# Performance work log

Hardware: AMD Instinct MI355X
Metric: run time of the kernel (lower is better)

The kernel has to match this reference:

```python
import jax, jax.numpy as jnp
import numpy as np

D = 1024      # d_model
H = 16        # nhead
DH = D // H   # d_head = 64
DC = D // 4   # d_compress = 256
HID = 2048    # dim_feedforward (SwiGLU hidden)
G = 2         # num_groups
EPG = 4       # experts_per_gp
E = G * EPG   # num_experts = 8
TOPK = 2
EPS = 1e-6
B, T = 2, 2048


def _rope_sincos(t, dh):
    inv_freq = 1.0 / (10000.0 ** (jnp.arange(0, dh, 2, dtype=jnp.float32) / dh))
    ang = jnp.arange(t, dtype=jnp.float32)[:, None] * inv_freq[None, :]  # [T, dh/2]
    return jnp.sin(ang), jnp.cos(ang)


def _apply_rope(x, sin, cos):
    # x: [B, H, T, DH]; sin/cos: [T, DH/2] broadcast over B,H
    x1 = x[..., ::2]
    x2 = x[..., 1::2]
    r = jnp.stack([x1 * cos - x2 * sin, x1 * sin + x2 * cos], axis=-1)
    return r.reshape(x.shape)


def _swiglu(x):
    a, b = jnp.split(x, 2, axis=-1)
    return jax.nn.silu(a) * b


def _rmsnorm(x, w):
    return x * jax.lax.rsqrt(jnp.mean(x * x, axis=-1, keepdims=True) + EPS) * w


def reference(src, Wq, Wk_c, Wv_c, Wk, Wv, Wo,
              W_shared_in, W_shared_out, W1_shared, W2_experts,
              Wg_gate, We_gate, group_bias, expert_bias, norm1_w, norm2_w):
    Bb, Tt, C = src.shape
    # ---- Latent attention (K/V compressed to d_c then re-expanded) ----
    q = (src @ Wq).reshape(Bb, Tt, H, DH).transpose(0, 2, 1, 3)
    k = ((src @ Wk_c) @ Wk).reshape(Bb, Tt, H, DH).transpose(0, 2, 1, 3)
    v = ((src @ Wv_c) @ Wv).reshape(Bb, Tt, H, DH).transpose(0, 2, 1, 3)
    sin, cos = _rope_sincos(Tt, DH)
    q = _apply_rope(q, sin, cos)
    k = _apply_rope(k, sin, cos)
    attn = jnp.einsum('bhqd,bhkd->bhqk', q, k) / np.sqrt(DH).astype(np.float32)
    attn = jax.nn.softmax(attn, axis=-1)
    sa = jnp.einsum('bhqk,bhkd->bhqd', attn, v)
    sa = sa.transpose(0, 2, 1, 3).reshape(Bb, Tt, C) @ Wo
    x = _rmsnorm(src + sa, norm1_w)

    # ---- Hierarchical MoE FFN ----
    S = Bb * Tt
    flat = x.reshape(S, C)
    shared = _swiglu(flat @ W_shared_in) @ W_shared_out          # [S, C]
    g_probs = jax.nn.softmax(flat @ Wg_gate + group_bias, -1)    # [S, G]
    g_idx = jnp.argmax(g_probs, axis=-1)                          # [S]
    e_logits = flat @ We_gate + expert_bias                       # [S, E]
    e_group = jnp.arange(E) // EPG
    in_group = e_group[None, :] == g_idx[:, None]                 # [S, E]
    e_probs = jax.nn.softmax(jnp.where(in_group, e_logits, -jnp.inf), -1)
    g_prob = jnp.take_along_axis(g_probs, g_idx[:, None], axis=1)  # [S, 1]
    p_expert = e_probs * g_prob
    topv, topi = jax.lax.top_k(p_expert, TOPK)                    # [S, K]
    # dense combine weights: zero for non-selected experts (same math as dispatch loop)
    w = jnp.zeros((S, E), flat.dtype).at[jnp.arange(S)[:, None], topi].set(topv)
    h = _swiglu(flat @ W1_shared)                                 # [S, HID] (w1 shared by all experts)
    routed = jnp.zeros_like(shared)
    for e in range(E):  # fixed small expert count
        routed = routed + (h @ W2_experts[e]) * w[:, e:e + 1]
    out = x + (shared + routed).reshape(Bb, Tt, C)
    return _rmsnorm(out, norm2_w)


def setup_inputs() -> dict:
    key = jax.random.key(0)
    ks = jax.random.split(key, 14)
    s = 0.02
    return {
        'src': jax.random.normal(ks[0], (B, T, D), jnp.float32),
        'Wq': jax.random.normal(ks[1], (D, D), jnp.float32) * s,
        'Wk_c': jax.random.normal(ks[2], (D, DC), jnp.float32) * s,
        'Wv_c': jax.random.normal(ks[3], (D, DC), jnp.float32) * s,
        'Wk': jax.random.normal(ks[4], (DC, D), jnp.float32) * s,
        'Wv': jax.random.normal(ks[5], (DC, D), jnp.float32) * s,
        'Wo': jax.random.normal(ks[6], (D, D), jnp.float32) * s,
        'W_shared_in': jax.random.normal(ks[7], (D, 2 * HID), jnp.float32) * s,
        'W_shared_out': jax.random.normal(ks[8], (HID, D), jnp.float32) * s,
        'W1_shared': jax.random.normal(ks[9], (D, 2 * HID), jnp.float32) * s,
        'W2_experts': jax.random.normal(ks[10], (E, HID, D), jnp.float32) * s,
        'Wg_gate': jax.random.normal(ks[11], (D, G), jnp.float32) * s,
        'We_gate': jax.random.normal(ks[12], (D, E), jnp.float32) * s,
        'group_bias': jnp.zeros((G,), jnp.float32),
        'expert_bias': jnp.zeros((E,), jnp.float32),
        'norm1_w': jnp.ones((D,), jnp.float32),
        'norm2_w': jnp.ones((D,), jnp.float32),
    }
```

## Files before the change

### kernel.cpp

```cpp
#include <hip/hip_runtime.h>
#include <math.h>

#define D_    1024
#define H_    16
#define DH_   64
#define DC_   256
#define HID_  2048
#define E_    8
#define B_    2
#define T_    2048
#define S_    4096
#define EPS_  1e-6f
#define QKVW_ 3072

typedef unsigned short u16;
typedef short bf16x8 __attribute__((ext_vector_type(8)));
typedef float f32x4 __attribute__((ext_vector_type(4)));

__device__ __forceinline__ float b2f(u16 u) {
    return __uint_as_float(((unsigned int)u) << 16);
}
__device__ __forceinline__ u16 f2b(float f) {
    unsigned int u = __float_as_uint(f);
    u += 0x7FFF + ((u >> 16) & 1);
    return (u16)(u >> 16);
}
__device__ __forceinline__ void g2l16(const u16* g, u16* l) {
    __builtin_amdgcn_global_load_lds(
        (const __attribute__((address_space(1))) void*)g,
        (__attribute__((address_space(3))) void*)l, 16, 0, 0);
}

__global__ __launch_bounds__(256) void conv_t(const float* __restrict__ in,
                                              u16* __restrict__ out,
                                              int K, int N,
                                              long inZ, long outZ, int perm) {
    in  += (long)blockIdx.z * inZ;
    out += (long)blockIdx.z * outZ;
    __shared__ float t[32][33];
    const int n0 = blockIdx.x * 32, k0 = blockIdx.y * 32;
    int src_n0 = n0;
    if (perm) {
        int t64 = n0 >> 6;
        src_n0 = ((n0 & 63) == 0) ? t64 * 32 : (N / 2 + t64 * 32);
    }
    const int tx = threadIdx.x & 31, ty = threadIdx.x >> 5;
#pragma unroll
    for (int i = 0; i < 4; i++)
        t[ty + 8 * i][tx] = in[(long)(k0 + ty + 8 * i) * N + src_n0 + tx];
    __syncthreads();
#pragma unroll
    for (int i = 0; i < 4; i++)
        out[(long)(n0 + ty + 8 * i) * K + k0 + tx] = f2b(t[tx][ty + 8 * i]);
}

__global__ __launch_bounds__(256) void vt_conv(const u16* __restrict__ qkv,
                                               u16* __restrict__ vt) {
    __shared__ u16 t[32][34];
    const int bh = blockIdx.z;
    const int b = bh >> 4, h = bh & 15;
    const int t0 = blockIdx.x * 32, d0 = blockIdx.y * 32;
    const int tx = threadIdx.x & 31, ty = threadIdx.x >> 5;
#pragma unroll
    for (int i = 0; i < 4; i++)
        t[ty + 8 * i][tx] =
            qkv[((long)b * T_ + t0 + ty + 8 * i) * QKVW_ + 2048 + h * 64 + d0 + tx];
    __syncthreads();
#pragma unroll
    for (int i = 0; i < 4; i++)
        vt[((long)bh * 64 + d0 + ty + 8 * i) * T_ + t0 + tx] = t[tx][ty + 8 * i];
}

__global__ __launch_bounds__(256) void convert_bf16(const float* __restrict__ in,
                                                    u16* __restrict__ out, int n4) {
    int i = blockIdx.x * 256 + threadIdx.x;
    if (i >= n4) return;
    float4 f = ((const float4*)in)[i];
    ushort4 o;
    o.x = f2b(f.x); o.y = f2b(f.y); o.z = f2b(f.z); o.w = f2b(f.w);
    ((ushort4*)out)[i] = o;
}

template<int OUTMODE>
__global__ __launch_bounds__(256) void gemm_bf16(const u16* __restrict__ A,
                                                 const u16* __restrict__ Bt,
                                                 void* __restrict__ Cp,
                                                 int N, int K, int ldo,
                                                 void* __restrict__ Cp2) {
    __shared__ u16 As[128 * 32];
    __shared__ u16 Bs[128 * 32];
    const int tid  = threadIdx.x;
    const int lane = tid & 63;
    const int wv   = tid >> 6;
    const int wm   = wv >> 1, wn = wv & 1;
    const long row0 = (long)blockIdx.y * 128;
    const long col0 = (long)blockIdx.x * 128;
    const int Klocal = K / gridDim.z;
    const long koff  = (long)blockIdx.z * Klocal;

    f32x4 acc[4][4];
#pragma unroll
    for (int i = 0; i < 4; i++)
#pragma unroll
        for (int j = 0; j < 4; j++) acc[i][j] = (f32x4){0.f, 0.f, 0.f, 0.f};

    const int sr = tid >> 2;
    const int sc = (tid & 3) << 3;
    const u16* Ag  = A  + (row0 + sr) * (long)K + koff + sc;
    const u16* Ag2 = Ag + 64 * (long)K;
    const u16* Bg  = Bt + (col0 + sr) * (long)K + koff + sc;
    const u16* Bg2 = Bg + 64 * (long)K;
    u16* lA  = As + tid * 8;
    u16* lA2 = As + 2048 + tid * 8;
    u16* lB  = Bs + tid * 8;
    u16* lB2 = Bs + 2048 + tid * 8;

    const int fl = lane & 15;
    const int fk = (lane >> 4) << 3;
    const u16* ArA = As + (wm * 64 + fl) * 32 + fk;
    const u16* BrB = Bs + (wn * 64 + fl) * 32 + fk;

    for (int k0 = 0; k0 < Klocal; k0 += 32) {
        __syncthreads();
        g2l16(Ag + k0, lA);
        g2l16(Ag2 + k0, lA2);
        g2l16(Bg + k0, lB);
        g2l16(Bg2 + k0, lB2);
        __syncthreads();
        bf16x8 af[4], bfr[4];
#pragma unroll
        for (int mi = 0; mi < 4; mi++) af[mi]  = *(const bf16x8*)(ArA + mi * 512);
#pragma unroll
        for (int ni = 0; ni < 4; ni++) bfr[ni] = *(const bf16x8*)(BrB + ni * 512);
#pragma unroll
        for (int mi = 0; mi < 4; mi++)
#pragma unroll
            for (int ni = 0; ni < 4; ni++)
                acc[mi][ni] = __builtin_amdgcn_mfma_f32_16x16x32_bf16(
                    af[mi], bfr[ni], acc[mi][ni], 0, 0, 0);
    }

    const int cr = (lane >> 4) << 2;
    const int cc = lane & 15;
#pragma unroll
    for (int mi = 0; mi < 4; mi++) {
#pragma unroll
        for (int r = 0; r < 4; r++) {
            long grow = row0 + wm * 64 + mi * 16 + cr + r;
            if (OUTMODE == 3) {
                u16* outb = (u16*)Cp + (long)(blockIdx.x >> 5) * S_ * HID_;
                u16* hrow = outb + grow * ldo + (blockIdx.x & 31) * 64 + wn * 32;
#pragma unroll
                for (int ni = 0; ni < 2; ni++) {
                    float a = acc[mi][ni][r], b = acc[mi][ni + 2][r];
                    float sig = 1.f / (1.f + __expf(-a));
                    hrow[ni * 16 + cc] = f2b(a * sig * b);
                }
            } else {
#pragma unroll
                for (int ni = 0; ni < 4; ni++) {
                    long gcol = col0 + wn * 64 + ni * 16 + cc;
                    float v = acc[mi][ni][r];
                    if (OUTMODE == 1)      ((u16*)Cp)[grow * ldo + gcol] = f2b(v);
                    else if (OUTMODE == 2) ((u16*)Cp)[gcol * ldo + grow] = f2b(v);
                    else {
                        float* basep = (float*)(blockIdx.z ? Cp2 : Cp);
                        basep[grow * ldo + gcol] = v;
                    }
                }
            }
        }
    }
}

__global__ __launch_bounds__(256) void routed_gemm(const u16* __restrict__ Hh,
                                                   const u16* __restrict__ W2T,
                                                   const int* __restrict__ list,
                                                   const float* __restrict__ wlist,
                                                   const int* __restrict__ bases,
                                                   const int* __restrict__ counts,
                                                   float* __restrict__ Cout) {
    const int e    = blockIdx.y >> 5;
    const int tile = blockIdx.y & 31;
    const int cnt  = counts[e];
    if (tile * 128 >= cnt) return;
    const int base = bases[e];

    __shared__ u16 As[128 * 32];
    __shared__ u16 Bs[128 * 32];
    __shared__ int   toks[128];
    __shared__ float wrow[128];

    const int tid = threadIdx.x;
    if (tid < 128) {
        int ridx = tile * 128 + tid;
        if (ridx < cnt) { toks[tid] = list[base + ridx]; wrow[tid] = wlist[base + ridx]; }
        else            { toks[tid] = -1;                wrow[tid] = 0.f; }
    }
    __syncthreads();

    const int lane = tid & 63;
    const int wv   = tid >> 6;
    const int wm   = wv >> 1, wn = wv & 1;
    const long col0 = (long)blockIdx.x * 128;

    f32x4 acc[4][4];
#pragma unroll
    for (int i = 0; i < 4; i++)
#pragma unroll
        for (int j = 0; j < 4; j++) acc[i][j] = (f32x4){0.f, 0.f, 0.f, 0.f};

    const int sr = tid >> 2;
    const int sc = (tid & 3) << 3;
    const int t1 = toks[sr], t2 = toks[sr + 64];
    const u16* Ag  = Hh + (long)(t1 < 0 ? 0 : t1) * HID_ + sc;
    const u16* Ag2 = Hh + (long)(t2 < 0 ? 0 : t2) * HID_ + sc;
    const u16* Bg  = W2T + (long)e * D_ * HID_ + (col0 + sr) * (long)HID_ + sc;
    const u16* Bg2 = Bg + 64 * (long)HID_;
    u16* lA  = As + tid * 8;
    u16* lA2 = As + 2048 + tid * 8;
    u16* lB  = Bs + tid * 8;
    u16* lB2 = Bs + 2048 + tid * 8;

    const int fl = lane & 15;
    const int fk = (lane >> 4) << 3;
    const u16* ArA = As + (wm * 64 + fl) * 32 + fk;
    const u16* BrB = Bs + (wn * 64 + fl) * 32 + fk;

    for (int k0 = 0; k0 < HID_; k0 += 32) {
        __syncthreads();
        g2l16(Ag + k0, lA);
        g2l16(Ag2 + k0, lA2);
        g2l16(Bg + k0, lB);
        g2l16(Bg2 + k0, lB2);
        __syncthreads();
        bf16x8 af[4], bfr[4];
#pragma unroll
        for (int mi = 0; mi < 4; mi++) af[mi]  = *(const bf16x8*)(ArA + mi * 512);
#pragma unroll
        for (int ni = 0; ni < 4; ni++) bfr[ni] = *(const bf16x8*)(BrB + ni * 512);
#pragma unroll
        for (int mi = 0; mi < 4; mi++)
#pragma unroll
            for (int ni = 0; ni < 4; ni++)
                acc[mi][ni] = __builtin_amdgcn_mfma_f32_16x16x32_bf16(
                    af[mi], bfr[ni], acc[mi][ni], 0, 0, 0);
    }

    const int cr = (lane >> 4) << 2;
    const int cc = lane & 15;
#pragma unroll
    for (int mi = 0; mi < 4; mi++) {
#pragma unroll
        for (int r = 0; r < 4; r++) {
            int rr = wm * 64 + mi * 16 + cr + r;
            int tk = toks[rr];
            if (tk < 0) continue;
            float wvw = wrow[rr];
            float* crow = Cout + (long)tk * D_ + col0 + wn * 64;
#pragma unroll
            for (int ni = 0; ni < 4; ni++)
                atomicAdd(crow + ni * 16 + cc, acc[mi][ni][r] * wvw);
        }
    }
}

__global__ __launch_bounds__(256) void rope_table(float2* __restrict__ tab) {
    int idx = blockIdx.x * 256 + threadIdx.x;
    int t = idx >> 5, i = idx & 31;
    float ang = (float)t * powf(10000.f, -(float)i / 32.f);
    float sn, cs;
    sincosf(ang, &sn, &cs);
    tab[idx] = make_float2(sn, cs);
}

__global__ __launch_bounds__(256) void rope_apply(u16* __restrict__ qkv,
                                                  const float2* __restrict__ tab) {
    long p = (long)blockIdx.x * 256 + threadIdx.x;
    int s  = (int)(p >> 8);
    int c8 = (int)(p & 255) << 3;
    int t  = s & (T_ - 1);
    const float2* tp = tab + t * 32 + ((c8 & 63) >> 1);
    u16* px = qkv + (long)s * QKVW_ + c8;
    bf16x8 v = *(const bf16x8*)px;
    bf16x8 o;
#pragma unroll
    for (int j = 0; j < 4; j++) {
        float x1 = b2f((u16)v[2 * j]), x2 = b2f((u16)v[2 * j + 1]);
        float2 sc = tp[j];
        o[2 * j]     = (short)f2b(x1 * sc.y - x2 * sc.x);
        o[2 * j + 1] = (short)f2b(x1 * sc.x + x2 * sc.y);
    }
    *(bf16x8*)px = o;
}

__global__ __launch_bounds__(512) void attn_kernel(const u16* __restrict__ qkv,
                                                   const u16* __restrict__ vtg,
                                                   u16* __restrict__ sab) {
    __shared__ u16 Ks[128 * 64];
    __shared__ u16 Vs[64 * 128];
    __shared__ u16 Ps[8][16 * 128];
    const int tid  = threadIdx.x;
    const int lane = tid & 63;
    const int w    = tid >> 6;
    const int bh = blockIdx.y;
    const int b  = bh >> 4, h = bh & 15;
    const long tok0 = (long)b * T_ + blockIdx.x * 128;
    const int fl = lane & 15;
    const int fq = lane >> 4;

    bf16x8 qf0, qf1;
    {
        const u16* qp = qkv + (tok0 + w * 16 + fl) * QKVW_ + h * 64 + fq * 8;
        qf0 = *(const bf16x8*)qp;
        qf1 = *(const bf16x8*)(qp + 32);
    }

    const u16* kb0 = qkv + ((long)b * T_) * QKVW_ + 1024 + h * 64;
    const u16* vb0 = vtg + ((long)bh * 64) * T_;

    float m_[4], l_[4];
    f32x4 oacc[4];
#pragma unroll
    for (int i = 0; i < 4; i++) {
        m_[i] = -1e30f; l_[i] = 0.f;
        oacc[i] = (f32x4){0.f, 0.f, 0.f, 0.f};
    }

    for (int kt = 0; kt < T_ / 128; kt++) {
        __syncthreads();
#pragma unroll
        for (int ps = 0; ps < 2; ps++) {
            int i = tid + ps * 512;
            int row = i >> 3, gg = i & 7;
            g2l16(kb0 + (long)(kt * 128 + row) * QKVW_ + ((gg ^ (row & 7)) << 3),
                  Ks + i * 8);
        }
#pragma unroll
        for (int ps = 0; ps < 2; ps++) {
            int i = tid + ps * 512;
            int row = i >> 4, gg = i & 15;
            g2l16(vb0 + (long)row * T_ + kt * 128 + ((gg ^ (row & 15)) << 3),
                  Vs + i * 8);
        }
        __syncthreads();

        f32x4 sacc[8];
#pragma unroll
        for (int ni = 0; ni < 8; ni++) sacc[ni] = (f32x4){0.f, 0.f, 0.f, 0.f};
#pragma unroll
        for (int ks = 0; ks < 2; ks++) {
            bf16x8 qq = ks ? qf1 : qf0;
#pragma unroll
            for (int ni = 0; ni < 8; ni++) {
                bf16x8 kf = *(const bf16x8*)(Ks + (ni * 16 + fl) * 64 +
                                             (((ks * 4 + fq) ^ (fl & 7)) << 3));
                sacc[ni] = __builtin_amdgcn_mfma_f32_16x16x32_bf16(qq, kf, sacc[ni], 0, 0, 0);
            }
        }

        float rmax[4];
#pragma unroll
        for (int r = 0; r < 4; r++) {
            float mm = sacc[0][r];
#pragma unroll
            for (int ni = 1; ni < 8; ni++) mm = fmaxf(mm, sacc[ni][r]);
            rmax[r] = mm * 0.125f;
        }
#pragma unroll
        for (int off = 1; off < 16; off <<= 1)
#pragma unroll
            for (int r = 0; r < 4; r++) rmax[r] = fmaxf(rmax[r], __shfl_xor(rmax[r], off));
        float alpha[4], psum[4];
#pragma unroll
        for (int r = 0; r < 4; r++) {
            float nm = fmaxf(m_[r], rmax[r]);
            alpha[r] = __expf(m_[r] - nm);
            m_[r] = nm;
            psum[r] = 0.f;
        }
        u16* pst = Ps[w];
#pragma unroll
        for (int ni = 0; ni < 8; ni++) {
            int colg = ni * 2 + (fl >> 3);
            int cl   = fl & 7;
#pragma unroll
            for (int r = 0; r < 4; r++) {
                int row = fq * 4 + r;
                float p = __expf(sacc[ni][r] * 0.125f - m_[r]);
                psum[r] += p;
                pst[row * 128 + ((colg ^ (row & 15)) << 3) + cl] = f2b(p);
            }
        }
#pragma unroll
        for (int off = 1; off < 16; off <<= 1)
#pragma unroll
            for (int r = 0; r < 4; r++) psum[r] += __shfl_xor(psum[r], off);
#pragma unroll
        for (int r = 0; r < 4; r++) l_[r] = l_[r] * alpha[r] + psum[r];
#pragma unroll
        for (int ni = 0; ni < 4; ni++)
#pragma unroll
            for (int r = 0; r < 4; r++) oacc[ni][r] *= alpha[r];

#pragma unroll
        for (int ks = 0; ks < 4; ks++) {
            bf16x8 pf = *(const bf16x8*)(pst + fl * 128 +
                                         (((ks * 4 + fq) ^ fl) << 3));
#pragma unroll
            for (int ni = 0; ni < 4; ni++) {
                bf16x8 vf = *(const bf16x8*)(Vs + (ni * 16 + fl) * 128 +
                                             (((ks * 4 + fq) ^ fl) << 3));
                oacc[ni] = __builtin_amdgcn_mfma_f32_16x16x32_bf16(pf, vf, oacc[ni], 0, 0, 0);
            }
        }
    }

#pragma unroll
    for (int r = 0; r < 4; r++) {
        float inv = 1.f / l_[r];
        u16* op = sab + (tok0 + w * 16 + fq * 4 + r) * D_ + h * 64 + fl;
#pragma unroll
        for (int ni = 0; ni < 4; ni++) op[ni * 16] = f2b(oacc[ni][r] * inv);
    }
}

template<int BF>
__global__ __launch_bounds__(256) void rmsnorm_res(const float* __restrict__ a,
                                                   const float* __restrict__ b,
                                                   const float* __restrict__ b2,
                                                   const float* __restrict__ w,
                                                   float* __restrict__ outf,
                                                   u16* __restrict__ outb) {
    const int s = blockIdx.x;
    const float* ar = a + (long)s * D_;
    const float* br = b + (long)s * D_;
    const float* cr2 = b2 + (long)s * D_;
    float y[4];
    float ss = 0.f;
#pragma unroll
    for (int kx = 0; kx < 4; kx++) {
        int j = threadIdx.x + kx * 256;
        y[kx] = ar[j] + br[j] + cr2[j];
        ss += y[kx] * y[kx];
    }
    __shared__ float red[4];
#pragma unroll
    for (int off = 32; off > 0; off >>= 1) ss += __shfl_down(ss, off);
    int lane = threadIdx.x & 63, wv = threadIdx.x >> 6;
    if (lane == 0) red[wv] = ss;
    __syncthreads();
    float tot = red[0] + red[1] + red[2] + red[3];
    float scl = rsqrtf(tot / (float)D_ + EPS_);
    float* orow = outf + (long)s * D_;
#pragma unroll
    for (int kx = 0; kx < 4; kx++) {
        int j = threadIdx.x + kx * 256;
        float v = y[kx] * scl * w[j];
        orow[j] = v;
        if (BF) outb[(long)s * D_ + j] = f2b(v);
    }
}

__global__ __launch_bounds__(256) void gate_kernel(const float* __restrict__ x,
                                                   const float* __restrict__ Wg,
                                                   const float* __restrict__ We,
                                                   const float* __restrict__ gb,
                                                   const float* __restrict__ eb,
                                                   int* __restrict__ tok_e,
                                                   float* __restrict__ tok_w) {
    const int wave = threadIdx.x >> 6;
    const int lane = threadIdx.x & 63;
    const int s = blockIdx.x * 4 + wave;
    const float* xr = x + (long)s * D_;
    float g0 = 0.f, g1 = 0.f;
    float ee[8];
#pragma unroll
    for (int e = 0; e < 8; e++) ee[e] = 0.f;
    for (int j = lane; j < D_; j += 64) {
        float xv = xr[j];
        g0 += xv * Wg[j * 2 + 0];
        g1 += xv * Wg[j * 2 + 1];
#pragma unroll
        for (int e = 0; e < 8; e++) ee[e] += xv * We[j * 8 + e];
    }
#pragma unroll
    for (int off = 32; off > 0; off >>= 1) {
        g0 += __shfl_down(g0, off);
        g1 += __shfl_down(g1, off);
#pragma unroll
        for (int e = 0; e < 8; e++) ee[e] += __shfl_down(ee[e], off);
    }
    if (lane == 0) {
        g0 += gb[0];
        g1 += gb[1];
        int gidx = (g1 > g0) ? 1 : 0;
        float gm = fmaxf(g0, g1);
        float p0 = expf(g0 - gm), p1 = expf(g1 - gm);
        float gprob = (gidx ? p1 : p0) / (p0 + p1);
        int base = gidx * 4;
        float pe[4];
        float em = -1e30f;
#pragma unroll
        for (int i = 0; i < 4; i++) {
            pe[i] = ee[base + i] + eb[base + i];
            em = fmaxf(em, pe[i]);
        }
        float sum = 0.f;
#pragma unroll
        for (int i = 0; i < 4; i++) { pe[i] = expf(pe[i] - em); sum += pe[i]; }
        float inv = gprob / sum;
#pragma unroll
        for (int i = 0; i < 4; i++) pe[i] *= inv;
        int i1 = 0;
        for (int i = 1; i < 4; i++) if (pe[i] > pe[i1]) i1 = i;
        int i2 = -1;
        for (int i = 0; i < 4; i++) {
            if (i == i1) continue;
            if (i2 < 0 || pe[i] > pe[i2]) i2 = i;
        }
        tok_e[s * 2 + 0] = base + i1;
        tok_e[s * 2 + 1] = base + i2;
        tok_w[s * 2 + 0] = pe[i1];
        tok_w[s * 2 + 1] = pe[i2];
    }
}

__global__ __launch_bounds__(256) void route_build(const int* __restrict__ tok_e,
                                                   const float* __restrict__ tok_w,
                                                   int* __restrict__ counts_g,
                                                   int* __restrict__ bases_g,
                                                   int* __restrict__ list,
                                                   float* __restrict__ wlist) {
    __shared__ int cnt[E_], bas[E_], cur[E_];
    const int tid = threadIdx.x;
    if (tid < E_) cnt[tid] = 0;
    __syncthreads();
    for (int i = tid; i < 2 * S_; i += 256) atomicAdd(&cnt[tok_e[i]], 1);
    __syncthreads();
    if (tid == 0) {
        int acc = 0;
        for (int e = 0; e < E_; e++) { bas[e] = acc; cur[e] = acc; acc += cnt[e]; }
    }
    __syncthreads();
    if (tid < E_) { counts_g[tid] = cnt[tid]; bases_g[tid] = bas[tid]; }
    for (int i = tid; i < 2 * S_; i += 256) {
        int e = tok_e[i];
        int p = atomicAdd(&cur[e], 1);
        list[p] = i >> 1;
        wlist[p] = tok_w[i];
    }
}

extern "C" void kernel_launch(void* const* d_in, const int* in_sizes, int n_in,
                              void* d_out, int out_size, void* d_ws, size_t ws_size,
                              hipStream_t stream) {
    const float* src  = (const float*)d_in[0];
    const float* Wq   = (const float*)d_in[1];
    const float* Wk_c = (const float*)d_in[2];
    const float* Wv_c = (const float*)d_in[3];
    const float* Wk   = (const float*)d_in[4];
    const float* Wv   = (const float*)d_in[5];
    const float* Wo   = (const float*)d_in[6];
    const float* Wsin = (const float*)d_in[7];
    const float* Wsout= (const float*)d_in[8];
    const float* W1   = (const float*)d_in[9];
    const float* W2   = (const float*)d_in[10];
    const float* Wg   = (const float*)d_in[11];
    const float* We   = (const float*)d_in[12];
    const float* gb   = (const float*)d_in[13];
    const float* eb   = (const float*)d_in[14];
    const float* n1w  = (const float*)d_in[15];
    const float* n2w  = (const float*)d_in[16];
    float* out = (float*)d_out;

    const size_t MB = 1u << 20;
    char* w8 = (char*)d_ws;
    u16*  qkv   = (u16*)(w8);
    u16*  vtg   = (u16*)(w8 + 24 * MB);
    float* oproj0 = (float*)(w8);
    float* oproj1 = (float*)(w8 + 16 * MB);
    u16*  w2t   = (u16*)(w8);
    u16*  WkcB  = (u16*)(w8 + 24 * MB);
    u16*  WvcB  = (u16*)(w8 + 24 * MB + 512 * 1024);
    u16*  WkTs  = (u16*)(w8 + 25 * MB);
    u16*  WvTs  = (u16*)(w8 + 25 * MB + 512 * 1024);
    u16*  sab   = (u16*)(w8 + 32 * MB);
    float* tokw = (float*)(w8 + 32 * MB);
    float* wlist = tokw + 2 * S_;
    int* toke   = (int*)(wlist + 2 * S_);
    int* list   = toke + 2 * S_;
    int* counts = list + 2 * S_;
    int* bases  = counts + E_;
    float* x1   = (float*)(w8 + 40 * MB);
    float* ffn0 = (float*)(w8 + 56 * MB);
    u16*  x1b   = (u16*)(w8 + 72 * MB);
    u16*  hbuf  = (u16*)(w8 + 80 * MB);
    u16*  srcb  = (u16*)(w8 + 96 * MB);
    float2* rtab= (float2*)(w8 + 104 * MB);
    u16*  hbuf2 = (u16*)(w8 + 96 * MB);
    u16*  WqkvT = (u16*)(w8 + 112 * MB);
    u16*  WsoutT= (u16*)(w8 + 112 * MB);
    u16*  WoT   = (u16*)(w8 + 118 * MB);
    u16*  WsinT = (u16*)(w8 + 120 * MB);
    u16*  W1T   = (u16*)(w8 + 128 * MB);
    float* ffn1 = (float*)(w8 + 120 * MB);

    dim3 blk(256);

    conv_t<<<dim3(32, 32), blk, 0, stream>>>(Wq, WqkvT, 1024, 1024, 0, 0, 0);
    convert_bf16<<<dim3(D_ * DC_ / 4 / 256), blk, 0, stream>>>(Wk_c, WkcB, D_ * DC_ / 4);
    convert_bf16<<<dim3(D_ * DC_ / 4 / 256), blk, 0, stream>>>(Wv_c, WvcB, D_ * DC_ / 4);
    conv_t<<<dim3(32, 8), blk, 0, stream>>>(Wk, WkTs, 256, 1024, 0, 0, 0);
    conv_t<<<dim3(32, 8), blk, 0, stream>>>(Wv, WvTs, 256, 1024, 0, 0, 0);
    gemm_bf16<2><<<dim3(8, 8), blk, 0, stream>>>(WkcB, WkTs, WqkvT + 1024 * 1024, 1024, 256, 1024, nullptr);
    gemm_bf16<2><<<dim3(8, 8), blk, 0, stream>>>(WvcB, WvTs, WqkvT + 2048 * 1024, 1024, 256, 1024, nullptr);

    convert_bf16<<<dim3(S_ * D_ / 4 / 256), blk, 0, stream>>>(src, srcb, S_ * D_ / 4);

    gemm_bf16<1><<<dim3(24, 32), blk, 0, stream>>>(srcb, WqkvT, qkv, QKVW_, 1024, QKVW_, nullptr);

    conv_t<<<dim3(32, 32), blk, 0, stream>>>(Wo, WoT, 1024, 1024, 0, 0, 0);
    conv_t<<<dim3(128, 32), blk, 0, stream>>>(Wsin, WsinT, 1024, 4096, 0, 0, 1);
    conv_t<<<dim3(32, 64), blk, 0, stream>>>(Wsout, WsoutT, 2048, 1024, 0, 0, 0);
    conv_t<<<dim3(128, 32), blk, 0, stream>>>(W1, W1T, 1024, 4096, 0, 0, 1);

    rope_table<<<dim3(T_ * 32 / 256), blk, 0, stream>>>(rtab);
    rope_apply<<<dim3(S_ * 2048 / 8 / 256), blk, 0, stream>>>(qkv, rtab);

    vt_conv<<<dim3(T_ / 32, 2, B_ * H_), blk, 0, stream>>>(qkv, vtg);
    attn_kernel<<<dim3(T_ / 128, B_ * H_), dim3(512), 0, stream>>>(qkv, vtg, sab);

    gemm_bf16<5><<<dim3(8, 32, 2), blk, 0, stream>>>(sab, WoT, oproj0, 1024, 1024, 1024, oproj1);
    rmsnorm_res<1><<<dim3(S_), blk, 0, stream>>>(src, oproj0, oproj1, n1w, x1, x1b);

    gemm_bf16<3><<<dim3(64, 32), blk, 0, stream>>>(x1b, WsinT, hbuf, 8192, 1024, 2048, nullptr);

    gemm_bf16<5><<<dim3(8, 32, 2), blk, 0, stream>>>(hbuf, WsoutT, ffn0, 1024, 2048, 1024, ffn1);

    gate_kernel<<<dim3(S_ / 4), blk, 0, stream>>>(x1, Wg, We, gb, eb, toke, tokw);
    route_build<<<dim3(1), blk, 0, stream>>>(toke, tokw, counts, bases, list, wlist);

    conv_t<<<dim3(32, 64, 8), blk, 0, stream>>>(W2, w2t, 2048, 1024,
                                                (long)HID_ * D_, (long)D_ * HID_, 0);
    routed_gemm<<<dim3(8, E_ * 32), blk, 0, stream>>>(hbuf2, w2t, list, wlist,
                                                      bases, counts, ffn0);

    rmsnorm_res<0><<<dim3(S_), blk, 0, stream>>>(x1, ffn0, ffn1, n2w, out, (u16*)nullptr);
}
```

Baseline: 670.5 us.

## Double-buffer K tiles, read V from global, swizzle block order in attention

Attention now double-buffers the K tile in shared memory, prefetching the next tile while the current one is computed. V fragments are read straight from global memory instead of being staged in LDS. The block index is remapped so that consecutive blocks fall on different heads, and s_setprio raises wave priority around the MFMA loops. The goal is to hide load latency and cut one barrier-bound staging step per tile, at the cost of uncached global V reads that may add memory latency inside the inner loop.

```diff
diff --git a/kernel.cpp b/kernel.cpp
--- a/kernel.cpp
+++ b/kernel.cpp
@@ -297,15 +297,17 @@
 __global__ __launch_bounds__(512) void attn_kernel(const u16* __restrict__ qkv,
                                                    const u16* __restrict__ vtg,
                                                    u16* __restrict__ sab) {
-    __shared__ u16 Ks[128 * 64];
-    __shared__ u16 Vs[64 * 128];
+    __shared__ u16 Ks[2][128 * 64];
     __shared__ u16 Ps[8][16 * 128];
     const int tid  = threadIdx.x;
     const int lane = tid & 63;
     const int w    = tid >> 6;
-    const int bh = blockIdx.y;
+    const int flat = blockIdx.x + (blockIdx.y << 4);
+    const int virt = ((flat & 7) << 6) | (flat >> 3);
+    const int qt = virt & 15;
+    const int bh = virt >> 4;
     const int b  = bh >> 4, h = bh & 15;
-    const long tok0 = (long)b * T_ + blockIdx.x * 128;
+    const long tok0 = (long)b * T_ + qt * 128;
     const int fl = lane & 15;
     const int fq = lane >> 4;
 
@@ -327,37 +329,38 @@
         oacc[i] = (f32x4){0.f, 0.f, 0.f, 0.f};
     }
 
-    for (int kt = 0; kt < T_ / 128; kt++) {
-        __syncthreads();
+    auto stageK = [&](int kt, int buf) {
 #pragma unroll
         for (int ps = 0; ps < 2; ps++) {
             int i = tid + ps * 512;
             int row = i >> 3, gg = i & 7;
             g2l16(kb0 + (long)(kt * 128 + row) * QKVW_ + ((gg ^ (row & 7)) << 3),
-                  Ks + i * 8);
-        }
-#pragma unroll
-        for (int ps = 0; ps < 2; ps++) {
-            int i = tid + ps * 512;
-            int row = i >> 4, gg = i & 15;
-            g2l16(vb0 + (long)row * T_ + kt * 128 + ((gg ^ (row & 15)) << 3),
-                  Vs + i * 8);
-        }
+                  Ks[buf] + i * 8);
+        }
+    };
+
+    stageK(0, 0);
+    int cur = 0;
+    for (int kt = 0; kt < T_ / 128; kt++) {
         __syncthreads();
+        if (kt + 1 < T_ / 128) stageK(kt + 1, cur ^ 1);
+        const u16* kbase = Ks[cur];
 
         f32x4 sacc[8];
 #pragma unroll
         for (int ni = 0; ni < 8; ni++) sacc[ni] = (f32x4){0.f, 0.f, 0.f, 0.f};
+        __builtin_amdgcn_s_setprio(1);
 #pragma unroll
         for (int ks = 0; ks < 2; ks++) {
             bf16x8 qq = ks ? qf1 : qf0;
 #pragma unroll
             for (int ni = 0; ni < 8; ni++) {
-                bf16x8 kf = *(const bf16x8*)(Ks + (ni * 16 + fl) * 64 +
+                bf16x8 kf = *(const bf16x8*)(kbase + (ni * 16 + fl) * 64 +
                                              (((ks * 4 + fq) ^ (fl & 7)) << 3));
                 sacc[ni] = __builtin_amdgcn_mfma_f32_16x16x32_bf16(qq, kf, sacc[ni], 0, 0, 0);
             }
         }
+        __builtin_amdgcn_s_setprio(0);
 
         float rmax[4];
 #pragma unroll
@@ -403,17 +406,21 @@
 #pragma unroll
             for (int r = 0; r < 4; r++) oacc[ni][r] *= alpha[r];
 
+        __builtin_amdgcn_s_setprio(1);
 #pragma unroll
         for (int ks = 0; ks < 4; ks++) {
             bf16x8 pf = *(const bf16x8*)(pst + fl * 128 +
                                          (((ks * 4 + fq) ^ fl) << 3));
 #pragma unroll
             for (int ni = 0; ni < 4; ni++) {
-                bf16x8 vf = *(const bf16x8*)(Vs + (ni * 16 + fl) * 128 +
-                                             (((ks * 4 + fq) ^ fl) << 3));
+                const u16* vp = vb0 + (long)(ni * 16 + fl) * T_ + kt * 128 +
+                                ((ks * 4 + fq) << 3);
+                bf16x8 vf = *(const bf16x8*)vp;
                 oacc[ni] = __builtin_amdgcn_mfma_f32_16x16x32_bf16(pf, vf, oacc[ni], 0, 0, 0);
             }
         }
+        __builtin_amdgcn_s_setprio(0);
+        cur ^= 1;
     }
 
 #pragma unroll
```

Result: slower. 761.3 us (+13.5%).
